# Performance work log

Hardware: AMD Instinct MI355X
Metric: run time of the kernel (lower is better)

Reference implementation:

```python
import jax, jax.numpy as jnp
import numpy as np

B, N, D, H = 8, 1024, 512, 8
DH = D // H  # 64
ALPHA = 0.2  # LeakyReLU slope (args.alpha)
EPS = 1e-6
NEG = -1e9


def layer_norm(x, g, b):
    mean = jnp.mean(x, axis=-1, keepdims=True)
    std = jnp.std(x, axis=-1, keepdims=True)
    return g * (x - mean) / (std + EPS) + b


def setup_inputs() -> dict:
    key = jax.random.key(0)
    ks = jax.random.split(key, 6)
    x = jax.random.normal(ks[0], (B, N, D), dtype=jnp.float32)
    mask = jnp.zeros((B, N), dtype=jnp.int32)  # unused by the block body
    adj = jax.random.randint(ks[1], (B, N, N), 0, 2).astype(jnp.int32)
    W = jax.random.normal(ks[2], (H, D, DH), dtype=jnp.float32) * 0.05
    a_src = jax.random.normal(ks[3], (H, DH), dtype=jnp.float32) * 0.05
    a_dst = jax.random.normal(ks[4], (H, DH), dtype=jnp.float32) * 0.05
    ln1_g = jnp.ones((D,), jnp.float32)
    ln1_b = jnp.zeros((D,), jnp.float32)
    ln2_g = jnp.ones((D,), jnp.float32)
    ln2_b = jnp.zeros((D,), jnp.float32)
    return {"x": x, "mask": mask, "adj": adj, "W": W, "a_src": a_src,
            "a_dst": a_dst, "ln1_g": ln1_g, "ln1_b": ln1_b,
            "ln2_g": ln2_g, "ln2_b": ln2_b}


def ggat(xn, adj, W, a_src, a_dst):
    # multi-head GAT-style attention over dense adjacency (inputP)
    h = jnp.einsum('bnd,hdk->bhnk', xn, W)                 # [B,H,N,DH]
    f_src = jnp.einsum('bhnk,hk->bhn', h, a_src)           # [B,H,N]
    f_dst = jnp.einsum('bhnk,hk->bhn', h, a_dst)
    e = jax.nn.leaky_relu(f_src[..., :, None] + f_dst[..., None, :], ALPHA)
    e = jnp.where(adj[:, None, :, :] > 0, e, NEG)          # mask non-edges
    attn = jax.nn.softmax(e, axis=-1)                      # [B,H,N,N]
    out = jnp.einsum('bhnm,bhmk->bhnk', attn, h)           # aggregate
    out = out.transpose(0, 2, 1, 3).reshape(out.shape[0], out.shape[2], -1)
    return jax.nn.elu(out)                                 # [B,N,D]


def reference(x, mask, adj, W, a_src, a_dst, ln1_g, ln1_b, ln2_g, ln2_b):
    # SublayerConnection: x + dropout(sublayer(norm(x))); dropout = identity (eval)
    xn = layer_norm(x, ln1_g, ln1_b)
    y = x + ggat(xn, adj, W, a_src, a_dst)
    # extra LayerNorm + dropout(identity); module returns (dropout(x), 0)
    y = layer_norm(y, ln2_g, ln2_b)
    return y
```

## Files before the change

kernel.cpp:

```cpp
#include <hip/hip_runtime.h>
#include <stdint.h>

#define B_ 8
#define N_ 1024
#define D_ 512
#define H_ 8
#define DH_ 64


using f16x8 = __attribute__((ext_vector_type(8))) _Float16;
using h2    = __attribute__((ext_vector_type(2))) _Float16;
using f32x4 = __attribute__((ext_vector_type(4))) float;

__device__ __forceinline__ float bf2f(uint32_t u) {
  union { uint32_t u; float f; } c; c.u = u << 16; return c.f;
}
__device__ __forceinline__ uint16_t f2bf(float f) {
  union { float f; uint32_t u; } c; c.f = f;
  return (uint16_t)((c.u + 0x7FFFu + ((c.u >> 16) & 1u)) >> 16);
}
__device__ __forceinline__ uint16_t f2h(float f) {
  union { _Float16 h; uint16_t u; } c; c.h = (_Float16)f; return c.u;
}
__device__ __forceinline__ float h2f(uint16_t u) {
  union { uint16_t u; _Float16 h; } c; c.u = u; return (float)c.h;
}
__device__ __forceinline__ uint32_t pk2h(float a, float b) {
  union { h2 h; uint32_t u; } c; c.h = (h2){(_Float16)a, (_Float16)b}; return c.u;
}
__device__ __forceinline__ h2 u2h2(uint32_t u) {
  union { uint32_t u; h2 h; } c; c.u = u; return c.h;
}
__device__ __forceinline__ uint32_t h22u(h2 h) {
  union { h2 h; uint32_t u; } c; c.h = h; return c.u;
}
__device__ __forceinline__ h2 h2splat(float v) {
  return (h2){(_Float16)v, (_Float16)v};
}
__device__ __forceinline__ h2 hmax2(h2 a, h2 b) {
#if defined(__has_builtin)
#if __has_builtin(__builtin_elementwise_max)
  return __builtin_elementwise_max(a, b);
#else
  h2 r; r.x = a.x > b.x ? a.x : b.x; r.y = a.y > b.y ? a.y : b.y; return r;
#endif
#else
  h2 r; r.x = a.x > b.x ? a.x : b.x; r.y = a.y > b.y ? a.y : b.y; return r;
#endif
}
__device__ __forceinline__ void load8f(const void* p, size_t idx, int f32, float v[8]) {
  if (f32) {
    const float4* q = (const float4*)((const float*)p + idx);
    float4 a = q[0], b = q[1];
    v[0]=a.x; v[1]=a.y; v[2]=a.z; v[3]=a.w; v[4]=b.x; v[5]=b.y; v[6]=b.z; v[7]=b.w;
  } else {
    uint4 u = *(const uint4*)((const uint16_t*)p + idx);
    const uint32_t* w = (const uint32_t*)&u;
#pragma unroll
    for (int e = 0; e < 4; e++) { v[2*e] = bf2f(w[e] & 0xffffu); v[2*e+1] = bf2f(w[e] >> 16); }
  }
}
__device__ __forceinline__ float load1f(const void* p, size_t idx, int f32) {
  return f32 ? ((const float*)p)[idx] : bf2f(((const uint16_t*)p)[idx]);
}

__device__ __forceinline__ int detect_f32_block(const uint16_t* x, int t, int* sflag) {
  if (t == 0) *sflag = 0;
  __syncthreads();
  uint2 u = ((const uint2*)x)[t];
  uint32_t bad = 0;
  bad |= (((u.x >> 7)  & 0xffu) >= 0x90u);
  bad |= (((u.x >> 23) & 0xffu) >= 0x90u);
  bad |= (((u.y >> 7)  & 0xffu) >= 0x90u);
  bad |= (((u.y >> 23) & 0xffu) >= 0x90u);
  if (__any(bad)) { if ((t & 63) == 0) atomicOr(sflag, 1); }
  __syncthreads();
  return *sflag;
}

__global__ __launch_bounds__(256) void k_pp(const int* __restrict__ adj,
                                            unsigned long long* __restrict__ adjp,
                                            const uint16_t* __restrict__ xr,
                                            int* __restrict__ flag,
                                            const void* __restrict__ x,
                                            const void* __restrict__ g,
                                            const void* __restrict__ bb,
                                            uint16_t* __restrict__ xn,
                                            const void* __restrict__ W,
                                            uint16_t* __restrict__ Wt) {
  const int bx = blockIdx.x, t = threadIdx.x;
  if (bx < 2048) {
    const int row  = bx * 4 + (t >> 6);
    const int lane = t & 63;
    const int* ar = adj + (size_t)row * N_;
#pragma unroll
    for (int c = 0; c < 16; c++) {
      unsigned long long m = __ballot(ar[c * 64 + lane] > 0);
      if (lane == 0) adjp[(size_t)row * 16 + c] = m;
    }
    return;
  }
  __shared__ int sflag;
  if (bx == 2048) {
    int f32 = detect_f32_block(xr, t, &sflag);
    if (t == 0) *flag = f32;
    return;
  }
  if (bx >= 4097) {
    const int f32 = detect_f32_block(xr, t, &sflag);
    const int bw = bx - 4097;
    const int h = bw >> 3, dt = bw & 7;
    __shared__ uint16_t tile[64][65];
    const size_t sbase = ((size_t)h * D_ + dt * 64) * DH_;
    for (int e = t; e < 4096; e += 256) tile[e >> 6][e & 63] = f2h(load1f(W, sbase + e, f32));
    __syncthreads();
    uint16_t* dst = Wt + (size_t)h * DH_ * D_ + dt * 64;
    for (int e = t; e < 4096; e += 256) {
      const int k = e >> 6, dd = e & 63;
      dst[(size_t)k * D_ + dd] = tile[dd][k];
    }
    return;
  }
  const int f32 = detect_f32_block(xr, t, &sflag);
  const int row  = (bx - 2049) * 4 + (t >> 6);
  const int lane = t & 63;
  const size_t base = (size_t)row * D_ + lane * 8;
  float v[8]; load8f(x, base, f32, v);
  float s = 0.f, sq = 0.f;
#pragma unroll
  for (int e = 0; e < 8; e++) { s += v[e]; sq += v[e] * v[e]; }
#pragma unroll
  for (int d = 32; d; d >>= 1) { s += __shfl_xor(s, d); sq += __shfl_xor(sq, d); }
  const float mean = s * (1.0f / D_);
  float var = fmaxf(sq * (1.0f / D_) - mean * mean, 0.0f);
  const float inv = 1.0f / (sqrtf(var) + 1e-6f);
  float gv[8], bv[8];
  load8f(g, lane * 8, f32, gv); load8f(bb, lane * 8, f32, bv);
  uint4 ov; uint32_t* ow = (uint32_t*)&ov;
#pragma unroll
  for (int e = 0; e < 4; e++) {
    float o0 = gv[2*e]   * ((v[2*e]   - mean) * inv) + bv[2*e];
    float o1 = gv[2*e+1] * ((v[2*e+1] - mean) * inv) + bv[2*e+1];
    ow[e] = (uint32_t)f2h(o0) | ((uint32_t)f2h(o1) << 16);
  }
  *(uint4*)(xn + base) = ov;
}

__global__ __launch_bounds__(256, 2) void k_gemm(const uint16_t* __restrict__ xn,
                                              const uint16_t* __restrict__ Wt,
                                              uint16_t* __restrict__ ht,
                                              const void* __restrict__ asr,
                                              const void* __restrict__ adst,
                                              float* __restrict__ fs,
                                              float* __restrict__ fd,
                                              const int* __restrict__ flag) {
  const int h = blockIdx.x;
  const int r0 = blockIdx.y * 64;
  const int t = threadIdx.x;
  const int wv = t >> 6, lane = t & 63, q = lane >> 4, m16 = lane & 15;
  const int wr = wv >> 1, wc = wv & 1;

  __shared__ union {
    struct { __align__(16) uint16_t A[64 * 72]; __align__(16) uint16_t Bt[64 * 72]; } st;
    __align__(16) uint16_t tr[64 * 72];
  } L;

  f32x4 acc[2][2] = {};
  const int srow = t >> 2, soff = (t & 3) * 16;
  const uint16_t* gA = xn + (size_t)(r0 + srow) * D_ + soff;
  const uint16_t* gB = Wt + ((size_t)h * DH_ + srow) * D_ + soff;
  uint16_t* lA = &L.st.A[srow * 72 + soff];
  uint16_t* lB = &L.st.Bt[srow * 72 + soff];

  uint4 va0 = *(const uint4*)(gA);
  uint4 va1 = *(const uint4*)(gA + 8);
  uint4 vb0 = *(const uint4*)(gB);
  uint4 vb1 = *(const uint4*)(gB + 8);
  for (int k0 = 0; k0 < D_; k0 += 64) {
    __syncthreads();
    *(uint4*)lA = va0;  *(uint4*)(lA + 8) = va1;
    *(uint4*)lB = vb0;  *(uint4*)(lB + 8) = vb1;
    __syncthreads();
    if (k0 + 64 < D_) {
      va0 = *(const uint4*)(gA + k0 + 64);
      va1 = *(const uint4*)(gA + k0 + 72);
      vb0 = *(const uint4*)(gB + k0 + 64);
      vb1 = *(const uint4*)(gB + k0 + 72);
    }
#pragma unroll
    for (int ks = 0; ks < 2; ks++) {
      f16x8 a0 = *(const f16x8*)&L.st.A[(wr * 32 + m16) * 72 + ks * 32 + q * 8];
      f16x8 a1 = *(const f16x8*)&L.st.A[(wr * 32 + 16 + m16) * 72 + ks * 32 + q * 8];
      f16x8 b0 = *(const f16x8*)&L.st.Bt[(wc * 32 + m16) * 72 + ks * 32 + q * 8];
      f16x8 b1 = *(const f16x8*)&L.st.Bt[(wc * 32 + 16 + m16) * 72 + ks * 32 + q * 8];
      acc[0][0] = __builtin_amdgcn_mfma_f32_16x16x32_f16(a0, b0, acc[0][0], 0, 0, 0);
      acc[0][1] = __builtin_amdgcn_mfma_f32_16x16x32_f16(a0, b1, acc[0][1], 0, 0, 0);
      acc[1][0] = __builtin_amdgcn_mfma_f32_16x16x32_f16(a1, b0, acc[1][0], 0, 0, 0);
      acc[1][1] = __builtin_amdgcn_mfma_f32_16x16x32_f16(a1, b1, acc[1][1], 0, 0, 0);
    }
  }
  __syncthreads();
#pragma unroll
  for (int i2 = 0; i2 < 2; i2++)
#pragma unroll
    for (int j2 = 0; j2 < 2; j2++) {
      f32x4 vv = acc[i2][j2];
      const int sl = wr * 32 + i2 * 16 + q * 4;
      const int kl = wc * 32 + j2 * 16 + m16;
#pragma unroll
      for (int r = 0; r < 4; r++) L.tr[kl * 72 + sl + r] = f2h(vv[r]);
    }
  __syncthreads();
  const int b = r0 >> 10, n0 = r0 & 1023;
  {
    const int k = t >> 2, ns = (t & 3) * 16;
    const size_t base = (((size_t)b * H_ + h) * DH_ + k) * (size_t)N_ + n0 + ns;
    *(uint4*)(ht + base) = *(const uint4*)&L.tr[k * 72 + ns];
    *(uint4*)(ht + base + 8) = *(const uint4*)&L.tr[k * 72 + ns + 8];
  }
  {
    const int f32 = *flag;
    const int nl = t >> 2, qd = (t & 3) * 16;
    float ss = 0.f, sd = 0.f;
#pragma unroll
    for (int dd = 0; dd < 16; dd++) {
      float hv = h2f(L.tr[(qd + dd) * 72 + nl]);
      ss = fmaf(hv, load1f(asr,  h * DH_ + qd + dd, f32), ss);
      sd = fmaf(hv, load1f(adst, h * DH_ + qd + dd, f32), sd);
    }
    ss += __shfl_xor(ss, 1); ss += __shfl_xor(ss, 2);
    sd += __shfl_xor(sd, 1); sd += __shfl_xor(sd, 2);
    if ((t & 3) == 0) {
      fs[((size_t)b * H_ + h) * N_ + n0 + nl] = ss;
      fd[((size_t)b * H_ + h) * N_ + n0 + nl] = sd;
    }
  }
}

__global__ __launch_bounds__(256, 2) void k_attn(const uint16_t* __restrict__ ht,
                                                 const float* __restrict__ fs,
                                                 const float* __restrict__ fd,
                                                 const uint32_t* __restrict__ adjp,
                                                 uint16_t* __restrict__ oat) {
  const int bid = blockIdx.x;
  const int bh = bid & 63, itile = bid >> 6;
  const int b = bh >> 3, h = bh & 7;
  const int i0 = itile * 128;
  const int t = threadIdx.x, wv = t >> 6, lane = t & 63, q = lane >> 4, m16 = lane & 15;
  __shared__ __align__(16) uint16_t Hs[64 * 136];
  __shared__ __align__(16) uint32_t E1p[N_ / 2];
  __shared__ __align__(16) uint32_t E2p[N_ / 2];
  for (int jp = t; jp < N_ / 2; jp += 256) {
    float2 fv = ((const float2*)(fd + (size_t)bh * N_))[jp];
    E1p[jp] = pk2h(exp2f(fv.x * 1.44269504f), exp2f(fv.y * 1.44269504f));
    E2p[jp] = pk2h(exp2f(fv.x * 0.28853901f), exp2f(fv.y * 0.28853901f));
  }
  const int iA0 = i0 + wv * 32 + m16;
  const int iA1 = iA0 + 16;
  const float fs0 = fs[(size_t)bh * N_ + iA0];
  const float fs1 = fs[(size_t)bh * N_ + iA1];
  const h2 Ea0 = h2splat(exp2f(fs0 * 1.44269504f));
  const h2 Eb0 = h2splat(exp2f(fs0 * 0.28853901f));
  const h2 Ea1 = h2splat(exp2f(fs1 * 1.44269504f));
  const h2 Eb1 = h2splat(exp2f(fs1 * 0.28853901f));
  const uint32_t* arow0 = adjp + ((size_t)b * N_ + iA0) * 32;
  const uint32_t* arow1 = adjp + ((size_t)b * N_ + iA1) * 32;
  const uint16_t* gH = ht + (size_t)bh * (DH_ * N_) + (size_t)(t >> 2) * N_ + (t & 3) * 32;
  uint16_t* lH = &Hs[(t >> 2) * 136 + (t & 3) * 32];
  union { uint16_t u[8]; f16x8 v; } ones;
#pragma unroll
  for (int e = 0; e < 8; e++) ones.u[e] = 0x3C00u;
  f32x4 acc[2][5] = {};
  uint4 v0 = *(const uint4*)(gH);
  uint4 v1 = *(const uint4*)(gH + 8);
  uint4 v2 = *(const uint4*)(gH + 16);
  uint4 v3 = *(const uint4*)(gH + 24);
  uint4 aw0 = *(const uint4*)(arow0);
  uint4 aw1 = *(const uint4*)(arow1);
  for (int c = 0; c < 8; c++) {
    __syncthreads();
    *(uint4*)(lH)      = v0;
    *(uint4*)(lH + 8)  = v1;
    *(uint4*)(lH + 16) = v2;
    *(uint4*)(lH + 24) = v3;
    __syncthreads();
    const uint32_t cw0[4] = {aw0.x, aw0.y, aw0.z, aw0.w};
    const uint32_t cw1[4] = {aw1.x, aw1.y, aw1.z, aw1.w};
    if (c < 7) {
      const int jn = (c + 1) * 128;
      v0 = *(const uint4*)(gH + jn);
      v1 = *(const uint4*)(gH + jn + 8);
      v2 = *(const uint4*)(gH + jn + 16);
      v3 = *(const uint4*)(gH + jn + 24);
      aw0 = *(const uint4*)(arow0 + (c + 1) * 4);
      aw1 = *(const uint4*)(arow1 + (c + 1) * 4);
    }
    const int eb = c * 64;
#pragma unroll
    for (int s = 0; s < 4; s++) {
      const int js = s * 32;
      f16x8 hf0 = *(const f16x8*)&Hs[(m16)      * 136 + js + q * 8];
      f16x8 hf1 = *(const f16x8*)&Hs[(16 + m16) * 136 + js + q * 8];
      f16x8 hf2 = *(const f16x8*)&Hs[(32 + m16) * 136 + js + q * 8];
      f16x8 hf3 = *(const f16x8*)&Hs[(48 + m16) * 136 + js + q * 8];
      const int ei = eb + s * 16 + q * 4;
      const uint4 e1u = *(const uint4*)&E1p[ei];
      const uint4 e2u = *(const uint4*)&E2p[ei];
      const h2 e1[4] = {u2h2(e1u.x), u2h2(e1u.y), u2h2(e1u.z), u2h2(e1u.w)};
      const h2 e2[4] = {u2h2(e2u.x), u2h2(e2u.y), u2h2(e2u.z), u2h2(e2u.w)};
      const uint32_t ab0 = (cw0[s] >> (q * 8)) & 0xffu;
      const uint32_t ab1 = (cw1[s] >> (q * 8)) & 0xffu;
      const uint32_t t0 = ab0 | (ab0 << 15);
      const uint32_t t1 = ab1 | (ab1 << 15);
#pragma unroll
      for (int f = 0; f < 2; f++) {
        const h2 Ea = f ? Ea1 : Ea0;
        const h2 Eb = f ? Eb1 : Eb0;
        const uint32_t tt = f ? t1 : t0;
        union { uint32_t u[4]; f16x8 v; } af;
#pragma unroll
        for (int p = 0; p < 4; p++) {
          h2 pm = hmax2(Ea * e1[p], Eb * e2[p]);
          af.u[p] = h22u(pm) & (((tt >> (2 * p)) & 0x10001u) * 0xFFFFu);
        }
        acc[f][0] = __builtin_amdgcn_mfma_f32_16x16x32_f16(af.v, hf0, acc[f][0], 0, 0, 0);
        acc[f][1] = __builtin_amdgcn_mfma_f32_16x16x32_f16(af.v, hf1, acc[f][1], 0, 0, 0);
        acc[f][2] = __builtin_amdgcn_mfma_f32_16x16x32_f16(af.v, hf2, acc[f][2], 0, 0, 0);
        acc[f][3] = __builtin_amdgcn_mfma_f32_16x16x32_f16(af.v, hf3, acc[f][3], 0, 0, 0);
        acc[f][4] = __builtin_amdgcn_mfma_f32_16x16x32_f16(af.v, ones.v, acc[f][4], 0, 0, 0);
      }
    }
  }
#pragma unroll
  for (int f = 0; f < 2; f++) {
    float linv[4];
#pragma unroll
    for (int r = 0; r < 4; r++) linv[r] = 1.0f / acc[f][4][r];
    const int ibl = i0 + wv * 32 + f * 16 + q * 4;
#pragma unroll
    for (int nt = 0; nt < 4; nt++)
#pragma unroll
      for (int r = 0; r < 4; r++) {
        oat[((size_t)b * N_ + ibl + r) * D_ + h * DH_ + nt * 16 + m16] =
            f2h(acc[f][nt][r] * linv[r]);
      }
  }
}

__global__ __launch_bounds__(256) void k_final(const void* __restrict__ x,
                                               const uint16_t* __restrict__ oa,
                                               const void* __restrict__ g,
                                               const void* __restrict__ bb,
                                               void* __restrict__ out,
                                               const int* __restrict__ flag) {
  const int f32 = *flag;
  const int row = blockIdx.x * 4 + (threadIdx.x >> 6);
  const int lane = threadIdx.x & 63;
  const size_t base = (size_t)row * D_ + lane * 8;
  float xv[8]; load8f(x, base, f32, xv);
  uint4 av = *(const uint4*)(oa + base);
  const uint32_t* aw = (const uint32_t*)&av;
  float v[8], s = 0.f, sq = 0.f;
#pragma unroll
  for (int e = 0; e < 4; e++) {
    float a0 = h2f((uint16_t)(aw[e] & 0xffffu));
    float a1 = h2f((uint16_t)(aw[e] >> 16));
    a0 = a0 > 0.f ? a0 : exp2f(a0 * 1.44269504f) - 1.0f;
    a1 = a1 > 0.f ? a1 : exp2f(a1 * 1.44269504f) - 1.0f;
    float t0 = xv[2*e] + a0, t1 = xv[2*e+1] + a1;
    v[2*e] = t0; v[2*e+1] = t1;
    s += t0 + t1; sq += t0 * t0 + t1 * t1;
  }
#pragma unroll
  for (int d = 32; d; d >>= 1) { s += __shfl_xor(s, d); sq += __shfl_xor(sq, d); }
  const float mean = s * (1.0f / D_);
  float var = fmaxf(sq * (1.0f / D_) - mean * mean, 0.0f);
  const float inv = 1.0f / (sqrtf(var) + 1e-6f);
  float gv[8], bv[8];
  load8f(g, lane * 8, f32, gv); load8f(bb, lane * 8, f32, bv);
  float r8[8];
#pragma unroll
  for (int e = 0; e < 8; e++) r8[e] = gv[e] * ((v[e] - mean) * inv) + bv[e];
  if (f32) {
    float* o = (float*)out + base;
    float4 o0 = {r8[0], r8[1], r8[2], r8[3]};
    float4 o1 = {r8[4], r8[5], r8[6], r8[7]};
    *(float4*)(o) = o0;
    *(float4*)(o + 4) = o1;
  } else {
    uint4 ov; uint32_t* ow = (uint32_t*)&ov;
#pragma unroll
    for (int e = 0; e < 4; e++)
      ow[e] = (uint32_t)f2bf(r8[2*e]) | ((uint32_t)f2bf(r8[2*e+1]) << 16);
    *(uint4*)((uint16_t*)out + base) = ov;
  }
}

extern "C" void kernel_launch(void* const* d_in, const int* in_sizes, int n_in,
                              void* d_out, int out_size, void* d_ws, size_t ws_size,
                              hipStream_t stream) {
  const void* x = d_in[0];
  const int* adj = (const int*)d_in[2];
  const void* W = d_in[3];
  const void* asr = d_in[4];
  const void* adst = d_in[5];
  const void* g1 = d_in[6];
  const void* b1 = d_in[7];
  const void* g2 = d_in[8];
  const void* b2 = d_in[9];

  uint8_t* ws = (uint8_t*)d_ws;
  uint16_t* ht = (uint16_t*)(ws);
  uint16_t* xn = (uint16_t*)(ws + 8388608);
  uint16_t* oat = xn;
  uint16_t* Wt = (uint16_t*)(ws + 16777216);
  uint32_t* adjp = (uint32_t*)(ws + 17301504);
  float* fs = (float*)(ws + 18350080);
  float* fd = (float*)(ws + 18612224);
  int* flag = (int*)(ws + 18874368);

  k_pp<<<dim3(4161), dim3(256), 0, stream>>>(adj, (unsigned long long*)adjp,
                                             (const uint16_t*)x, flag,
                                             x, g1, b1, xn, W, Wt);
  k_gemm<<<dim3(8, 128), dim3(256), 0, stream>>>(xn, Wt, ht, asr, adst, fs, fd, flag);
  k_attn<<<dim3(512), dim3(256), 0, stream>>>(ht, fs, fd, adjp, oat);
  k_final<<<dim3(2048), dim3(256), 0, stream>>>(x, oat, g2, b2, d_out, flag);
}
```

Measured before the change: 162.0 us.

## Double-buffer LDS tiles in GEMM and attention, use direct global-to-LDS loads

```diff
diff --git a/kernel.cpp b/kernel.cpp
--- a/kernel.cpp
+++ b/kernel.cpp
@@ -47,6 +47,11 @@
 #else
   h2 r; r.x = a.x > b.x ? a.x : b.x; r.y = a.y > b.y ? a.y : b.y; return r;
 #endif
+}
+__device__ __forceinline__ void gload16(const void* g, void* l) {
+  __builtin_amdgcn_global_load_lds(
+      (const __attribute__((address_space(1))) uint32_t*)g,
+      (__attribute__((address_space(3))) uint32_t*)l, 16, 0, 0);
 }
 __device__ __forceinline__ void load8f(const void* p, size_t idx, int f32, float v[8]) {
   if (f32) {
@@ -161,43 +166,47 @@
   const int wr = wv >> 1, wc = wv & 1;
 
   __shared__ union {
-    struct { __align__(16) uint16_t A[64 * 72]; __align__(16) uint16_t Bt[64 * 72]; } st;
+    struct { __align__(16) uint16_t A[2][64 * 72]; __align__(16) uint16_t Bt[2][64 * 72]; } st;
     __align__(16) uint16_t tr[64 * 72];
   } L;
 
   f32x4 acc[2][2] = {};
   const int srow = t >> 2, soff = (t & 3) * 16;
+  const int o = srow * 72 + soff;
   const uint16_t* gA = xn + (size_t)(r0 + srow) * D_ + soff;
   const uint16_t* gB = Wt + ((size_t)h * DH_ + srow) * D_ + soff;
-  uint16_t* lA = &L.st.A[srow * 72 + soff];
-  uint16_t* lB = &L.st.Bt[srow * 72 + soff];
 
   uint4 va0 = *(const uint4*)(gA);
   uint4 va1 = *(const uint4*)(gA + 8);
   uint4 vb0 = *(const uint4*)(gB);
   uint4 vb1 = *(const uint4*)(gB + 8);
+  *(uint4*)&L.st.A[0][o]      = va0;  *(uint4*)&L.st.A[0][o + 8]  = va1;
+  *(uint4*)&L.st.Bt[0][o]     = vb0;  *(uint4*)&L.st.Bt[0][o + 8] = vb1;
+  va0 = *(const uint4*)(gA + 64);  va1 = *(const uint4*)(gA + 72);
+  vb0 = *(const uint4*)(gB + 64);  vb1 = *(const uint4*)(gB + 72);
+  int cur = 0;
   for (int k0 = 0; k0 < D_; k0 += 64) {
     __syncthreads();
-    *(uint4*)lA = va0;  *(uint4*)(lA + 8) = va1;
-    *(uint4*)lB = vb0;  *(uint4*)(lB + 8) = vb1;
-    __syncthreads();
     if (k0 + 64 < D_) {
-      va0 = *(const uint4*)(gA + k0 + 64);
-      va1 = *(const uint4*)(gA + k0 + 72);
-      vb0 = *(const uint4*)(gB + k0 + 64);
-      vb1 = *(const uint4*)(gB + k0 + 72);
+      *(uint4*)&L.st.A[cur ^ 1][o]      = va0;  *(uint4*)&L.st.A[cur ^ 1][o + 8]  = va1;
+      *(uint4*)&L.st.Bt[cur ^ 1][o]     = vb0;  *(uint4*)&L.st.Bt[cur ^ 1][o + 8] = vb1;
+      if (k0 + 128 < D_) {
+        va0 = *(const uint4*)(gA + k0 + 128);  va1 = *(const uint4*)(gA + k0 + 136);
+        vb0 = *(const uint4*)(gB + k0 + 128);  vb1 = *(const uint4*)(gB + k0 + 136);
+      }
     }
 #pragma unroll
     for (int ks = 0; ks < 2; ks++) {
-      f16x8 a0 = *(const f16x8*)&L.st.A[(wr * 32 + m16) * 72 + ks * 32 + q * 8];
-      f16x8 a1 = *(const f16x8*)&L.st.A[(wr * 32 + 16 + m16) * 72 + ks * 32 + q * 8];
-      f16x8 b0 = *(const f16x8*)&L.st.Bt[(wc * 32 + m16) * 72 + ks * 32 + q * 8];
-      f16x8 b1 = *(const f16x8*)&L.st.Bt[(wc * 32 + 16 + m16) * 72 + ks * 32 + q * 8];
+      f16x8 a0 = *(const f16x8*)&L.st.A[cur][(wr * 32 + m16) * 72 + ks * 32 + q * 8];
+      f16x8 a1 = *(const f16x8*)&L.st.A[cur][(wr * 32 + 16 + m16) * 72 + ks * 32 + q * 8];
+      f16x8 b0 = *(const f16x8*)&L.st.Bt[cur][(wc * 32 + m16) * 72 + ks * 32 + q * 8];
+      f16x8 b1 = *(const f16x8*)&L.st.Bt[cur][(wc * 32 + 16 + m16) * 72 + ks * 32 + q * 8];
       acc[0][0] = __builtin_amdgcn_mfma_f32_16x16x32_f16(a0, b0, acc[0][0], 0, 0, 0);
       acc[0][1] = __builtin_amdgcn_mfma_f32_16x16x32_f16(a0, b1, acc[0][1], 0, 0, 0);
       acc[1][0] = __builtin_amdgcn_mfma_f32_16x16x32_f16(a1, b0, acc[1][0], 0, 0, 0);
       acc[1][1] = __builtin_amdgcn_mfma_f32_16x16x32_f16(a1, b1, acc[1][1], 0, 0, 0);
     }
+    cur ^= 1;
   }
   __syncthreads();
 #pragma unroll
@@ -247,9 +256,28 @@
   const int b = bh >> 3, h = bh & 7;
   const int i0 = itile * 128;
   const int t = threadIdx.x, wv = t >> 6, lane = t & 63, q = lane >> 4, m16 = lane & 15;
-  __shared__ __align__(16) uint16_t Hs[64 * 136];
+  __shared__ __align__(16) uint16_t Hs[2][64 * 128];
   __shared__ __align__(16) uint32_t E1p[N_ / 2];
   __shared__ __align__(16) uint32_t E2p[N_ / 2];
+
+  const uint16_t* hbase = ht + (size_t)bh * (DH_ * N_);
+  int srow[4], soff[4];
+#pragma unroll
+  for (int i = 0; i < 4; i++) {
+    const int r = wv * 16 + i * 4 + (lane >> 4);
+    srow[i] = r;
+    soff[i] = ((lane & 15) * 8) ^ ((r & 7) << 3);
+  }
+#define STAGE(jc, buf)                                                         \
+  {                                                                            \
+    _Pragma("unroll")                                                          \
+    for (int ii = 0; ii < 4; ii++) {                                           \
+      gload16(hbase + (size_t)srow[ii] * N_ + (jc) + soff[ii],                 \
+              &(buf)[(wv * 16 + ii * 4) * 128]);                               \
+    }                                                                          \
+  }
+  STAGE(0, Hs[0]);
+
   for (int jp = t; jp < N_ / 2; jp += 256) {
     float2 fv = ((const float2*)(fd + (size_t)bh * N_))[jp];
     E1p[jp] = pk2h(exp2f(fv.x * 1.44269504f), exp2f(fv.y * 1.44269504f));
@@ -257,52 +285,36 @@
   }
   const int iA0 = i0 + wv * 32 + m16;
   const int iA1 = iA0 + 16;
-  const float fs0 = fs[(size_t)bh * N_ + iA0];
-  const float fs1 = fs[(size_t)bh * N_ + iA1];
-  const h2 Ea0 = h2splat(exp2f(fs0 * 1.44269504f));
-  const h2 Eb0 = h2splat(exp2f(fs0 * 0.28853901f));
-  const h2 Ea1 = h2splat(exp2f(fs1 * 1.44269504f));
-  const h2 Eb1 = h2splat(exp2f(fs1 * 0.28853901f));
+  const h2 R0 = h2splat(fminf(exp2f(fs[(size_t)bh * N_ + iA0] * -1.15415603f), 60000.f));
+  const h2 R1 = h2splat(fminf(exp2f(fs[(size_t)bh * N_ + iA1] * -1.15415603f), 60000.f));
   const uint32_t* arow0 = adjp + ((size_t)b * N_ + iA0) * 32;
   const uint32_t* arow1 = adjp + ((size_t)b * N_ + iA1) * 32;
-  const uint16_t* gH = ht + (size_t)bh * (DH_ * N_) + (size_t)(t >> 2) * N_ + (t & 3) * 32;
-  uint16_t* lH = &Hs[(t >> 2) * 136 + (t & 3) * 32];
   union { uint16_t u[8]; f16x8 v; } ones;
 #pragma unroll
   for (int e = 0; e < 8; e++) ones.u[e] = 0x3C00u;
   f32x4 acc[2][5] = {};
-  uint4 v0 = *(const uint4*)(gH);
-  uint4 v1 = *(const uint4*)(gH + 8);
-  uint4 v2 = *(const uint4*)(gH + 16);
-  uint4 v3 = *(const uint4*)(gH + 24);
+  const int csw = (m16 & 7) << 3;
   uint4 aw0 = *(const uint4*)(arow0);
   uint4 aw1 = *(const uint4*)(arow1);
   for (int c = 0; c < 8; c++) {
     __syncthreads();
-    *(uint4*)(lH)      = v0;
-    *(uint4*)(lH + 8)  = v1;
-    *(uint4*)(lH + 16) = v2;
-    *(uint4*)(lH + 24) = v3;
-    __syncthreads();
+    if (c < 7) STAGE((c + 1) * 128, Hs[(c + 1) & 1]);
     const uint32_t cw0[4] = {aw0.x, aw0.y, aw0.z, aw0.w};
     const uint32_t cw1[4] = {aw1.x, aw1.y, aw1.z, aw1.w};
     if (c < 7) {
-      const int jn = (c + 1) * 128;
-      v0 = *(const uint4*)(gH + jn);
-      v1 = *(const uint4*)(gH + jn + 8);
-      v2 = *(const uint4*)(gH + jn + 16);
-      v3 = *(const uint4*)(gH + jn + 24);
       aw0 = *(const uint4*)(arow0 + (c + 1) * 4);
       aw1 = *(const uint4*)(arow1 + (c + 1) * 4);
     }
+    const uint16_t* Hc = Hs[c & 1];
     const int eb = c * 64;
 #pragma unroll
     for (int s = 0; s < 4; s++) {
       const int js = s * 32;
-      f16x8 hf0 = *(const f16x8*)&Hs[(m16)      * 136 + js + q * 8];
-      f16x8 hf1 = *(const f16x8*)&Hs[(16 + m16) * 136 + js + q * 8];
-      f16x8 hf2 = *(const f16x8*)&Hs[(32 + m16) * 136 + js + q * 8];
-      f16x8 hf3 = *(const f16x8*)&Hs[(48 + m16) * 136 + js + q * 8];
+      const int jb = (js + q * 8) ^ csw;
+      f16x8 hf0 = *(const f16x8*)&Hc[(m16)*128      + jb];
+      f16x8 hf1 = *(const f16x8*)&Hc[(16 + m16)*128 + jb];
+      f16x8 hf2 = *(const f16x8*)&Hc[(32 + m16)*128 + jb];
+      f16x8 hf3 = *(const f16x8*)&Hc[(48 + m16)*128 + jb];
       const int ei = eb + s * 16 + q * 4;
       const uint4 e1u = *(const uint4*)&E1p[ei];
       const uint4 e2u = *(const uint4*)&E2p[ei];
@@ -314,13 +326,12 @@
       const uint32_t t1 = ab1 | (ab1 << 15);
 #pragma unroll
       for (int f = 0; f < 2; f++) {
-        const h2 Ea = f ? Ea1 : Ea0;
-        const h2 Eb = f ? Eb1 : Eb0;
+        const h2 Rf = f ? R1 : R0;
         const uint32_t tt = f ? t1 : t0;
         union { uint32_t u[4]; f16x8 v; } af;
 #pragma unroll
         for (int p = 0; p < 4; p++) {
-          h2 pm = hmax2(Ea * e1[p], Eb * e2[p]);
+          h2 pm = hmax2(e1[p], Rf * e2[p]);
           af.u[p] = h22u(pm) & (((tt >> (2 * p)) & 0x10001u) * 0xFFFFu);
         }
         acc[f][0] = __builtin_amdgcn_mfma_f32_16x16x32_f16(af.v, hf0, acc[f][0], 0, 0, 0);
@@ -331,6 +342,7 @@
       }
     }
   }
+#undef STAGE
 #pragma unroll
   for (int f = 0; f < 2; f++) {
     float linv[4];
```

After: 157.6 us. 1.03x faster.
